# Kernel tuning notes

Measured on AMD Instinct MI355X. Metric: run time of the kernel, lower is better.

## Reference

```python
import jax, jax.numpy as jnp
import numpy as np

M, OUT, IN = 512, 8192, 8192
BLOCK_N, BLOCK_K = 128, 128  # weight_block_size (out_block, in_block)
OB, IB = OUT // BLOCK_N, IN // BLOCK_K  # 64, 64 scale blocks


def setup_inputs() -> dict:
    key = jax.random.key(0)
    k1, k2, k3 = jax.random.split(key, 3)
    x = jax.random.normal(k1, (M, IN), dtype=jnp.float32)
    # pre-quantized int8 weight stored as (out_features, in_features)
    weight_q = jax.random.randint(k2, (OUT, IN), -127, 127, dtype=jnp.int32).astype(jnp.int8)
    # per-(out_block, in_block) dequant scales
    weight_scale = jax.random.uniform(k3, (OB, IB), dtype=jnp.float32, minval=0.01, maxval=0.02)
    return {"x": x, "weight_q": weight_q, "weight_scale": weight_scale}


def _dequant(weight_q, weight_scale):
    # (OUT, IN) int8 -> blocks (OB, BLOCK_N, IB, BLOCK_K), scale broadcast per block
    w = weight_q.astype(jnp.float32).reshape(OB, BLOCK_N, IB, BLOCK_K)
    w = w * weight_scale[:, None, :, None]
    return w.reshape(OUT, IN)


def reference(x, weight_q, weight_scale):
    # Block-dequantize then matmul: out[m, o] = sum_i x[m, i] * (wq[o, i] * scale[o//bn, i//bk])
    w = _dequant(weight_q, weight_scale)          # (OUT, IN) fp32
    out = jnp.einsum("mi,oi->mo", x, w)           # (M, OUT)
    return out
```

## Files before the change

kernel.cpp:

```cpp
#include <hip/hip_runtime.h>

#define MDIM 512
#define NDIM 8192
#define KDIM 8192

typedef float v4f __attribute__((ext_vector_type(4)));
typedef int   v4i __attribute__((ext_vector_type(4)));
typedef char  c16 __attribute__((ext_vector_type(16)));

#define GLDS16(g, l)                                                    \
  __builtin_amdgcn_global_load_lds(                                     \
      (const __attribute__((address_space(1))) void*)(g),               \
      (__attribute__((address_space(3))) void*)(l), 16, 0, 0)
#define SB __builtin_amdgcn_sched_barrier(0)

__device__ __forceinline__ int swb(int row, int g) {
  return ((row >> 1) << 7) + (((((row & 1) << 2) | g) ^ ((row >> 1) & 7)) << 4);
}

__global__ __launch_bounds__(256) void produce_kernel(
    const int* __restrict__ wq, const float* __restrict__ x,
    char* __restrict__ w8, char* __restrict__ xq, float* __restrict__ ax) {
  if (blockIdx.x < 16384) {
    const int tid = blockIdx.x * 256 + threadIdx.x;
    const int R = tid >> 9;
    const int k16 = tid & 511;
    const int* src = wq + ((size_t)R << 13) + k16 * 16;
    v4i a[4];
#pragma unroll
    for (int h = 0; h < 4; ++h) a[h] = *(const v4i*)(src + h * 4);
    c16 q;
#pragma unroll
    for (int h = 0; h < 4; ++h) {
      q[h * 4 + 0] = (char)a[h][0];
      q[h * 4 + 1] = (char)a[h][1];
      q[h * 4 + 2] = (char)a[h][2];
      q[h * 4 + 3] = (char)a[h][3];
    }
    const int nt = R >> 6, r = R & 63;
    const int kt = k16 >> 2, g = k16 & 3;
    *(c16*)(w8 + ((size_t)(nt * 128 + kt) << 12) + swb(r, g)) = q;
  } else {
    const int m = blockIdx.x - 16384;
    const int t = threadIdx.x;
    const float* row = x + ((size_t)m << 13);
    v4f v[8];
    float mx = 0.f;
#pragma unroll
    for (int i = 0; i < 8; ++i) {
      v[i] = *(const v4f*)(row + t * 32 + i * 4);
#pragma unroll
      for (int r = 0; r < 4; ++r) mx = fmaxf(mx, fabsf(v[i][r]));
    }
#pragma unroll
    for (int d = 1; d < 64; d <<= 1) mx = fmaxf(mx, __shfl_xor(mx, d));
    __shared__ float smx[4];
    if ((t & 63) == 0) smx[t >> 6] = mx;
    __syncthreads();
    mx = fmaxf(fmaxf(smx[0], smx[1]), fmaxf(smx[2], smx[3]));
    const float inv = (mx > 0.f) ? 127.f / mx : 0.f;
    if (t == 0) ax[m] = mx / 127.f;
    const int mt = m >> 7, r = m & 127;
#pragma unroll
    for (int g2 = 0; g2 < 2; ++g2) {
      c16 q;
#pragma unroll
      for (int e = 0; e < 16; ++e) {
        const int idx = g2 * 4 + (e >> 2);
        float f = fminf(fmaxf(v[idx][e & 3] * inv, -127.f), 127.f);
        q[e] = (char)__float2int_rn(f);
      }
      const int k16 = t * 2 + g2;
      const int kt = k16 >> 2, g = k16 & 3;
      *(c16*)(xq + ((size_t)(mt * 128 + kt) << 13) + swb(r, g)) = q;
    }
  }
}

__global__ __launch_bounds__(256, 2) void gemm_i8_kernel(
    const char* __restrict__ xq, const char* __restrict__ w8,
    const float* __restrict__ wsc, const float* __restrict__ ax,
    float* __restrict__ out) {
  constexpr int NKT = 128;
  __shared__ char lA[3][8192];
  __shared__ char lB[3][4096];

  const int b = blockIdx.x;
  const int c = b & 7;
  const int s = b >> 3;
  const int mt = s & 3;
  const int nt = c * 16 + (s >> 2);
  const int m0 = mt * 128, n0 = nt * 64;

  const int t = threadIdx.x;
  const int w = t >> 6, l = t & 63;
  const int wm = (w >> 1) * 64, wn = (w & 1) * 32;
  const int l15 = l & 15, q = l >> 4;

  const char* asrc = xq + ((size_t)(mt * 128) << 13);
  const char* bsrc = w8 + ((size_t)(nt * 128) << 12);

  v4i acc[4][2] = {};
  v4f facc[4][2] = {};

  auto issue = [&](int tt) {
    const int buf = tt % 3;
#pragma unroll
    for (int it = 0; it < 2; ++it) {
      const int ub = (it * 4 + w) * 64;
      GLDS16(asrc + ((size_t)tt << 13) + (size_t)(ub + l) * 16, &lA[buf][ub * 16]);
    }
    GLDS16(bsrc + ((size_t)tt << 12) + (size_t)(w * 64 + l) * 16, &lB[buf][w * 1024]);
  };

  issue(0);
  issue(1);
#pragma unroll 1
  for (int tt = 0; tt < NKT; ++tt) {
    const int cur = tt % 3;
    SB;
    __builtin_amdgcn_s_barrier();
    SB;
    if (tt + 2 < NKT) {
      issue(tt + 2);
      SB;
      asm volatile("s_waitcnt vmcnt(6)" ::: "memory");
    } else if (tt + 1 < NKT) {
      asm volatile("s_waitcnt vmcnt(3)" ::: "memory");
    } else {
      asm volatile("s_waitcnt vmcnt(0)" ::: "memory");
    }
    SB;
    __builtin_amdgcn_s_barrier();
    SB;

    v4i af[4], bq[2];
#pragma unroll
    for (int i = 0; i < 4; ++i)
      af[i] = *(const v4i*)&lA[cur][swb(wm + i * 16 + l15, q)];
#pragma unroll
    for (int j = 0; j < 2; ++j)
      bq[j] = *(const v4i*)&lB[cur][swb(wn + j * 16 + l15, q)];
#pragma unroll
    for (int i = 0; i < 4; ++i)
#pragma unroll
      for (int j = 0; j < 2; ++j)
        acc[i][j] = __builtin_amdgcn_mfma_i32_16x16x64_i8(
            af[i], bq[j], acc[i][j], 0, 0, 0);

    if (tt & 1) {
      const float sc = wsc[(nt >> 1) * 64 + (tt >> 1)];
#pragma unroll
      for (int i = 0; i < 4; ++i)
#pragma unroll
        for (int j = 0; j < 2; ++j) {
#pragma unroll
          for (int r = 0; r < 4; ++r)
            facc[i][j][r] = fmaf(sc, (float)acc[i][j][r], facc[i][j][r]);
          acc[i][j] = v4i{0, 0, 0, 0};
        }
    }
  }

#pragma unroll
  for (int i = 0; i < 4; ++i) {
    const int mrow = m0 + wm + i * 16 + (l >> 4) * 4;
#pragma unroll
    for (int j = 0; j < 2; ++j) {
      const int ocol = n0 + wn + j * 16 + l15;
#pragma unroll
      for (int r = 0; r < 4; ++r)
        out[(size_t)(mrow + r) * NDIM + ocol] = ax[mrow + r] * facc[i][j][r];
    }
  }
}

extern "C" void kernel_launch(void* const* d_in, const int* in_sizes, int n_in,
                              void* d_out, int out_size, void* d_ws,
                              size_t ws_size, hipStream_t stream) {
  const float* x = (const float*)d_in[0];
  const int* wq = (const int*)d_in[1];
  const float* wsc = (const float*)d_in[2];
  float* out = (float*)d_out;

  const size_t W8 = (size_t)NDIM * KDIM;
  const size_t XQ = (size_t)MDIM * KDIM;

  char* w8 = (char*)d_ws;
  char* xq = (char*)d_ws + W8;
  float* ax = (float*)((char*)d_ws + W8 + XQ);

  produce_kernel<<<dim3(16384 + MDIM), dim3(256), 0, stream>>>(wq, x, w8, xq, ax);
  gemm_i8_kernel<<<dim3(512), dim3(256), 0, stream>>>(xq, w8, wsc, ax, out);
}
```

Before: 154.4 us.

## Retile int8 GEMM to 64x128 blocks with 512 threads and double buffering

Changes the GEMM block tile from 128x64 to 64x128 (M x N), raises the block to 512 threads (8 waves of 32x32), and loads two 64-wide K sub-tiles per phase so each 128-K scale block is one pipeline stage. The activation layout in the producer becomes 64-row tiles to match. Buffering drops from triple to double, and the per-block scale is applied once per phase. It aims to cut per-iteration barrier and waitcnt overhead and improve wave-level parallelism, at the cost of a shallower prefetch and one block per CU.

```diff
diff --git a/kernel.cpp b/kernel.cpp
--- a/kernel.cpp
+++ b/kernel.cpp
@@ -37,9 +37,9 @@
       q[h * 4 + 2] = (char)a[h][2];
       q[h * 4 + 3] = (char)a[h][3];
     }
-    const int nt = R >> 6, r = R & 63;
+    const int ntile = R >> 6, r = R & 63;
     const int kt = k16 >> 2, g = k16 & 3;
-    *(c16*)(w8 + ((size_t)(nt * 128 + kt) << 12) + swb(r, g)) = q;
+    *(c16*)(w8 + ((size_t)(ntile * 128 + kt) << 12) + swb(r, g)) = q;
   } else {
     const int m = blockIdx.x - 16384;
     const int t = threadIdx.x;
@@ -60,7 +60,7 @@
     mx = fmaxf(fmaxf(smx[0], smx[1]), fmaxf(smx[2], smx[3]));
     const float inv = (mx > 0.f) ? 127.f / mx : 0.f;
     if (t == 0) ax[m] = mx / 127.f;
-    const int mt = m >> 7, r = m & 127;
+    const int mt = m >> 6, r = m & 63;
 #pragma unroll
     for (int g2 = 0; g2 < 2; ++g2) {
       c16 q;
@@ -72,99 +72,108 @@
       }
       const int k16 = t * 2 + g2;
       const int kt = k16 >> 2, g = k16 & 3;
-      *(c16*)(xq + ((size_t)(mt * 128 + kt) << 13) + swb(r, g)) = q;
+      *(c16*)(xq + ((size_t)(mt * 128 + kt) << 12) + swb(r, g)) = q;
     }
   }
 }
 
-__global__ __launch_bounds__(256, 2) void gemm_i8_kernel(
+__global__ __launch_bounds__(512, 1) void gemm_i8_kernel(
     const char* __restrict__ xq, const char* __restrict__ w8,
     const float* __restrict__ wsc, const float* __restrict__ ax,
     float* __restrict__ out) {
-  constexpr int NKT = 128;
-  __shared__ char lA[3][8192];
-  __shared__ char lB[3][4096];
+  constexpr int NPH = 64;
+  __shared__ char lA[2][8192];
+  __shared__ char lB[2][16384];
 
   const int b = blockIdx.x;
   const int c = b & 7;
   const int s = b >> 3;
-  const int mt = s & 3;
-  const int nt = c * 16 + (s >> 2);
-  const int m0 = mt * 128, n0 = nt * 64;
+  const int mt = s & 7;
+  const int nt2 = c * 8 + (s >> 3);
+  const int m0 = mt * 64, n0 = nt2 * 128;
 
   const int t = threadIdx.x;
   const int w = t >> 6, l = t & 63;
-  const int wm = (w >> 1) * 64, wn = (w & 1) * 32;
+  const int wm = (w >> 2) * 32;
+  const int wn = (w & 3) * 32;
   const int l15 = l & 15, q = l >> 4;
 
-  const char* asrc = xq + ((size_t)(mt * 128) << 13);
-  const char* bsrc = w8 + ((size_t)(nt * 128) << 12);
-
-  v4i acc[4][2] = {};
-  v4f facc[4][2] = {};
+  v4i acc[2][2] = {};
+  v4f facc[2][2] = {};
 
   auto issue = [&](int tt) {
-    const int buf = tt % 3;
-#pragma unroll
-    for (int it = 0; it < 2; ++it) {
-      const int ub = (it * 4 + w) * 64;
-      GLDS16(asrc + ((size_t)tt << 13) + (size_t)(ub + l) * 16, &lA[buf][ub * 16]);
-    }
-    GLDS16(bsrc + ((size_t)tt << 12) + (size_t)(w * 64 + l) * 16, &lB[buf][w * 1024]);
+    const int buf = tt & 1;
+#pragma unroll
+    for (int it = 0; it < 3; ++it) {
+      const int u = w * 3 + it;
+      const int reg = u >> 2, qt = u & 3;
+      const char* src;
+      if (reg < 2) {
+        src = xq + ((size_t)(mt * 128 + tt * 2 + reg) << 12);
+      } else {
+        const int nh = (reg - 2) >> 1, kh = (reg - 2) & 1;
+        src = w8 + ((size_t)((nt2 * 2 + nh) * 128 + tt * 2 + kh) << 12);
+      }
+      src += qt * 1024 + (size_t)l * 16;
+      if (reg < 2)
+        GLDS16(src, &lA[buf][reg * 4096 + qt * 1024]);
+      else
+        GLDS16(src, &lB[buf][(reg - 2) * 4096 + qt * 1024]);
+    }
   };
 
   issue(0);
-  issue(1);
 #pragma unroll 1
-  for (int tt = 0; tt < NKT; ++tt) {
-    const int cur = tt % 3;
+  for (int tt = 0; tt < NPH; ++tt) {
+    const int cur = tt & 1;
     SB;
     __builtin_amdgcn_s_barrier();
     SB;
-    if (tt + 2 < NKT) {
-      issue(tt + 2);
-      SB;
-      asm volatile("s_waitcnt vmcnt(6)" ::: "memory");
-    } else if (tt + 1 < NKT) {
+    if (tt + 1 < NPH) issue(tt + 1);
+    SB;
+    if (tt + 1 < NPH)
       asm volatile("s_waitcnt vmcnt(3)" ::: "memory");
-    } else {
+    else
       asm volatile("s_waitcnt vmcnt(0)" ::: "memory");
-    }
     SB;
     __builtin_amdgcn_s_barrier();
     SB;
 
-    v4i af[4], bq[2];
-#pragma unroll
-    for (int i = 0; i < 4; ++i)
-      af[i] = *(const v4i*)&lA[cur][swb(wm + i * 16 + l15, q)];
-#pragma unroll
-    for (int j = 0; j < 2; ++j)
-      bq[j] = *(const v4i*)&lB[cur][swb(wn + j * 16 + l15, q)];
-#pragma unroll
-    for (int i = 0; i < 4; ++i)
-#pragma unroll
-      for (int j = 0; j < 2; ++j)
-        acc[i][j] = __builtin_amdgcn_mfma_i32_16x16x64_i8(
-            af[i], bq[j], acc[i][j], 0, 0, 0);
-
-    if (tt & 1) {
-      const float sc = wsc[(nt >> 1) * 64 + (tt >> 1)];
-#pragma unroll
-      for (int i = 0; i < 4; ++i)
-#pragma unroll
-        for (int j = 0; j < 2; ++j) {
-#pragma unroll
-          for (int r = 0; r < 4; ++r)
-            facc[i][j][r] = fmaf(sc, (float)acc[i][j][r], facc[i][j][r]);
-          acc[i][j] = v4i{0, 0, 0, 0};
-        }
-    }
+#pragma unroll
+    for (int kk = 0; kk < 2; ++kk) {
+      v4i af[2], bq[2];
+#pragma unroll
+      for (int i = 0; i < 2; ++i)
+        af[i] = *(const v4i*)&lA[cur][kk * 4096 + swb(wm + i * 16 + l15, q)];
+#pragma unroll
+      for (int j = 0; j < 2; ++j) {
+        const int rb = wn + j * 16 + l15;
+        bq[j] = *(const v4i*)&lB[cur][(rb >> 6) * 8192 + kk * 4096 +
+                                      swb(rb & 63, q)];
+      }
+#pragma unroll
+      for (int i = 0; i < 2; ++i)
+#pragma unroll
+        for (int j = 0; j < 2; ++j)
+          acc[i][j] = __builtin_amdgcn_mfma_i32_16x16x64_i8(
+              af[i], bq[j], acc[i][j], 0, 0, 0);
+    }
+
+    const float sc = wsc[nt2 * 64 + tt];
+#pragma unroll
+    for (int i = 0; i < 2; ++i)
+#pragma unroll
+      for (int j = 0; j < 2; ++j) {
+#pragma unroll
+        for (int r = 0; r < 4; ++r)
+          facc[i][j][r] = fmaf(sc, (float)acc[i][j][r], facc[i][j][r]);
+        acc[i][j] = v4i{0, 0, 0, 0};
+      }
   }
 
 #pragma unroll
-  for (int i = 0; i < 4; ++i) {
-    const int mrow = m0 + wm + i * 16 + (l >> 4) * 4;
+  for (int i = 0; i < 2; ++i) {
+    const int mrow = m0 + wm + i * 16 + q * 4;
 #pragma unroll
     for (int j = 0; j < 2; ++j) {
       const int ocol = n0 + wn + j * 16 + l15;
@@ -191,5 +200,5 @@
   float* ax = (float*)((char*)d_ws + W8 + XQ);
 
   produce_kernel<<<dim3(16384 + MDIM), dim3(256), 0, stream>>>(wq, x, w8, xq, ax);
-  gemm_i8_kernel<<<dim3(512), dim3(256), 0, stream>>>(xq, w8, wsc, ax, out);
-}
+  gemm_i8_kernel<<<dim3(512), dim3(512), 0, stream>>>(xq, w8, wsc, ax, out);
+}
```

After: 128.3 us. 16.9% less time.
